# Kernel tuning notes

Measured on AMD Instinct MI355X. Metric: run time of the kernel, lower is better.

Reference implementation:

```python
import jax, jax.numpy as jnp
import numpy as np
import math

EPS = 1e-8
DIM, HEADS, K = 256, 8, 16
HD = DIM // HEADS
B, N, PDIM = 4, 4096, 3


def _layernorm(x, w, b, eps=1e-5):
    m = jnp.mean(x, axis=-1, keepdims=True)
    v = jnp.mean((x - m) ** 2, axis=-1, keepdims=True)
    return (x - m) * jax.lax.rsqrt(v + eps) * w + b


def setup_inputs() -> dict:
    key = jax.random.key(0)
    ks = jax.random.split(key, 16)
    s = 0.02
    d = {
        'x': jax.random.normal(ks[0], (B, N, DIM), jnp.float32),
        'positions': jax.random.uniform(ks[1], (B, N, PDIM), jnp.float32) * 0.5,  # inside unit ball
        'c': jnp.ones((1,), jnp.float32),
        'time_emb': jax.random.normal(ks[2], (B, DIM), jnp.float32),
        'Wq': jax.random.normal(ks[3], (DIM, DIM), jnp.float32) * s,
        'bq': jnp.zeros((DIM,), jnp.float32),
        'Wk': jax.random.normal(ks[4], (DIM, DIM), jnp.float32) * s,
        'bk': jnp.zeros((DIM,), jnp.float32),
        'Wv': jax.random.normal(ks[5], (DIM, DIM), jnp.float32) * s,
        'bv': jnp.zeros((DIM,), jnp.float32),
        'Wo': jax.random.normal(ks[6], (DIM, DIM), jnp.float32) * s,
        'bo': jnp.zeros((DIM,), jnp.float32),
        'W1': jax.random.normal(ks[7], (DIM, 4 * DIM), jnp.float32) * s,
        'b1': jnp.zeros((4 * DIM,), jnp.float32),
        'W2': jax.random.normal(ks[8], (4 * DIM, DIM), jnp.float32) * s,
        'b2': jnp.zeros((DIM,), jnp.float32),
        'ln1_w': jnp.ones((DIM,), jnp.float32),
        'ln1_b': jnp.zeros((DIM,), jnp.float32),
        'ln2_w': jnp.ones((DIM,), jnp.float32),
        'ln2_b': jnp.zeros((DIM,), jnp.float32),
        'log_tau': jnp.zeros((), jnp.float32),
    }
    return d


def _poincare_dist_matrix(pos, c):
    # pos: [B,N,P], c: scalar > 0. Returns [B,N,N] with d[b,i,j] = dist(pos[b,j], pos[b,i])
    sq = jnp.sum(pos ** 2, axis=-1)                      # [B,N]
    diff2 = (sq[:, :, None] + sq[:, None, :]
             - 2.0 * jnp.einsum('bip,bjp->bij', pos, pos))
    diff2 = jnp.maximum(diff2, 0.0)
    num = 2.0 * c * diff2
    den = (1.0 - c * sq[:, :, None]) * (1.0 - c * sq[:, None, :])
    arg = jnp.maximum(1.0 + num / (den + EPS), 1.0)
    return jnp.arccosh(arg) / jnp.sqrt(c)


def reference(x, positions, c, time_emb, Wq, bq, Wk, bk, Wv, bv, Wo, bo,
              W1, b1, W2, b2, ln1_w, ln1_b, ln2_w, ln2_b, log_tau):
    c_s = jnp.squeeze(c)
    x_res = x
    h = _layernorm(x, ln1_w, ln1_b) + time_emb[:, None, :]

    q = (h @ Wq + bq).reshape(B, N, HEADS, HD).transpose(0, 2, 1, 3)  # [B,H,N,hd]
    k = (h @ Wk + bk).reshape(B, N, HEADS, HD).transpose(0, 2, 1, 3)
    v = (h @ Wv + bv).reshape(B, N, HEADS, HD).transpose(0, 2, 1, 3)

    # pairwise hyperbolic distances + kNN (no_grad in original)
    dist = jax.lax.stop_gradient(_poincare_dist_matrix(positions, c_s))  # [B,N,N]
    neg_vals, idx = jax.lax.top_k(-dist, K)          # smallest-K distances
    attn_dists = -neg_vals                            # [B,N,K]

    # gather neighbor keys/values: out[b,h,n,j,d] = k[b,h,idx[b,n,j],d]
    idx_flat = idx.reshape(B, 1, N * K, 1)            # broadcast over heads, hd
    k_g = jnp.take_along_axis(k, idx_flat, axis=2).reshape(B, HEADS, N, K, HD)
    v_g = jnp.take_along_axis(v, idx_flat, axis=2).reshape(B, HEADS, N, K, HD)

    feat = jnp.einsum('bhnd,bhnkd->bhnk', q, k_g) / math.sqrt(HD)
    tau = jnp.exp(log_tau) + EPS
    scores = feat - attn_dists[:, None, :, :] / tau
    probs = jax.nn.softmax(scores, axis=-1)
    attn = jnp.einsum('bhnk,bhnkd->bhnd', probs, v_g)
    attn = attn.transpose(0, 2, 1, 3).reshape(B, N, DIM)

    x2 = x_res + attn @ Wo + bo
    ff = jax.nn.gelu(_layernorm(x2, ln2_w, ln2_b) @ W1 + b1, approximate=False) @ W2 + b2
    return x2 + ff
```

## Files before the change

kernel.cpp:

```cpp
#include <hip/hip_runtime.h>
#include <math.h>

namespace {

constexpr int kBatch = 4;
constexpr int kN = 4096;
constexpr int kDim = 256;
constexpr int kHeads = 8;
constexpr int kK = 16;
constexpr float kEps = 1e-8f;

using u16 = unsigned short;
typedef __attribute__((ext_vector_type(8))) short short8;
typedef __attribute__((ext_vector_type(8))) u16 u16x8;
typedef __attribute__((ext_vector_type(4))) float f32x4;

__device__ __forceinline__ float b2f(u16 u) {
  union { unsigned int i; float f; } x; x.i = ((unsigned int)u) << 16; return x.f;
}
__device__ __forceinline__ u16 f2b(float f) {
  union { float f; unsigned int i; } x; x.f = f;
  unsigned int r = x.i + 0x7fffu + ((x.i >> 16) & 1u);
  return (u16)(r >> 16);
}
__device__ __forceinline__ float gelu_exact(float x) {
  return 0.5f * x * (1.0f + erff(x * 0.70710678118654752f));
}
__device__ __forceinline__ void load_lds16(const u16* g, u16* l) {
  __builtin_amdgcn_global_load_lds(
      (const __attribute__((address_space(1))) unsigned int*)g,
      (__attribute__((address_space(3))) unsigned int*)l, 16, 0, 0);
}

template<bool ADD_TEMB>
__global__ __launch_bounds__(256) void ln_kernel(
    const float* __restrict__ x, const float* __restrict__ w,
    const float* __restrict__ bb, const float* __restrict__ temb,
    u16* __restrict__ out) {
  int gt = blockIdx.x * 256 + threadIdx.x;
  int row = gt >> 6;
  int lane = threadIdx.x & 63;
  const float4* xr = (const float4*)(x + (size_t)row * kDim);
  float4 v = xr[lane];
  float s = v.x + v.y + v.z + v.w;
  #pragma unroll
  for (int off = 32; off; off >>= 1) s += __shfl_xor(s, off);
  float mean = s * (1.0f / kDim);
  float dx = v.x - mean, dy = v.y - mean, dz = v.z - mean, dw = v.w - mean;
  float ss = dx * dx + dy * dy + dz * dz + dw * dw;
  #pragma unroll
  for (int off = 32; off; off >>= 1) ss += __shfl_xor(ss, off);
  float rstd = rsqrtf(ss * (1.0f / kDim) + 1e-5f);
  float4 wv = ((const float4*)w)[lane];
  float4 bv = ((const float4*)bb)[lane];
  float ox = dx * rstd * wv.x + bv.x;
  float oy = dy * rstd * wv.y + bv.y;
  float oz = dz * rstd * wv.z + bv.z;
  float ow = dw * rstd * wv.w + bv.w;
  if (ADD_TEMB) {
    int bi = row >> 12;
    float4 t = ((const float4*)(temb + (size_t)bi * kDim))[lane];
    ox += t.x; oy += t.y; oz += t.z; ow += t.w;
  }
  ushort4 ob;
  ob.x = f2b(ox); ob.y = f2b(oy); ob.z = f2b(oz); ob.w = f2b(ow);
  ((ushort4*)(out + (size_t)row * kDim))[lane] = ob;
}

__global__ __launch_bounds__(256) void wtrans_kernel(
    const float* __restrict__ Wq, const float* __restrict__ Wk,
    const float* __restrict__ Wv, const float* __restrict__ Wo,
    const float* __restrict__ W1, const float* __restrict__ W2,
    u16* __restrict__ Tq, u16* __restrict__ Tk,
    u16* __restrict__ Tv, u16* __restrict__ To,
    u16* __restrict__ T1, u16* __restrict__ T2) {
  __shared__ float t[32][33];
  int bx = blockIdx.x;
  int seg = bx >> 8, e = bx & 255;
  const float* W; u16* T; int Kin, Nin, kt, nt;
  if (seg == 0) {
    int which = e >> 6, tl = e & 63;
    W = which == 0 ? Wq : which == 1 ? Wk : which == 2 ? Wv : Wo;
    T = which == 0 ? Tq : which == 1 ? Tk : which == 2 ? Tv : To;
    Kin = 256; Nin = 256; kt = tl >> 3; nt = tl & 7;
  } else if (seg == 1) {
    W = W1; T = T1; Kin = 256; Nin = 1024; kt = e >> 5; nt = e & 31;
  } else {
    W = W2; T = T2; Kin = 1024; Nin = 256; kt = e >> 3; nt = e & 7;
  }
  int tx = threadIdx.x & 31, ty = threadIdx.x >> 5;
  #pragma unroll
  for (int rr = 0; rr < 4; ++rr) {
    int r = rr * 8 + ty;
    t[r][tx] = W[(size_t)(kt * 32 + r) * Nin + nt * 32 + tx];
  }
  __syncthreads();
  #pragma unroll
  for (int rr = 0; rr < 4; ++rr) {
    int r = rr * 8 + ty;
    T[(size_t)(nt * 32 + r) * Kin + kt * 32 + tx] = f2b(t[tx][r]);
  }
}

template<int EPI, int BN>
__device__ __forceinline__ void gemm_body(
    const u16* __restrict__ A, const u16* __restrict__ Bt,
    const float* __restrict__ bias, const float* __restrict__ R,
    float* __restrict__ Cf, u16* __restrict__ Cbf,
    int N, int K, int bx, int by) {
  constexpr int NI = BN / 32;
  constexpr int BK = 64;
  __shared__ u16 Al[128 * BK];
  __shared__ u16 Bl[BN * BK];
  int tid = threadIdx.x;
  int wv = tid >> 6, ln = tid & 63;
  int wr = wv >> 1, wc = wv & 1;
  int lhi = ln >> 4, llo = ln & 15;
  int bm = bx * 128, bn = by * BN;

  f32x4 zero = {0.f, 0.f, 0.f, 0.f};
  f32x4 acc[4][NI];
  #pragma unroll
  for (int mi = 0; mi < 4; ++mi)
    #pragma unroll
    for (int ni = 0; ni < NI; ++ni) acc[mi][ni] = zero;

  for (int k0 = 0; k0 < K; k0 += BK) {
    if (k0) __syncthreads();
    #pragma unroll
    for (int i = 0; i < 128 * BK / (8 * 256); ++i) {
      int f = i * 256 + tid;
      int r = f >> 3, o = f & 7;
      load_lds16(A + (size_t)(bm + r) * K + k0 + ((o ^ (r & 7)) << 3),
                 &Al[(i * 256 + wv * 64) * 8]);
    }
    #pragma unroll
    for (int i = 0; i < BN * BK / (8 * 256); ++i) {
      int f = i * 256 + tid;
      int r = f >> 3, o = f & 7;
      load_lds16(Bt + (size_t)(bn + r) * K + k0 + ((o ^ (r & 7)) << 3),
                 &Bl[(i * 256 + wv * 64) * 8]);
    }
    __syncthreads();
    #pragma unroll
    for (int ks = 0; ks < BK; ks += 32) {
      short8 af[4], bf[NI];
      #pragma unroll
      for (int mi = 0; mi < 4; ++mi) {
        int row = wr * 64 + mi * 16 + llo;
        int oct = ((ks >> 3) + lhi) ^ (llo & 7);
        af[mi] = *(const short8*)&Al[row * BK + oct * 8];
      }
      #pragma unroll
      for (int ni = 0; ni < NI; ++ni) {
        int row = wc * (BN / 2) + ni * 16 + llo;
        int oct = ((ks >> 3) + lhi) ^ (llo & 7);
        bf[ni] = *(const short8*)&Bl[row * BK + oct * 8];
      }
      #pragma unroll
      for (int mi = 0; mi < 4; ++mi)
        #pragma unroll
        for (int ni = 0; ni < NI; ++ni)
          acc[mi][ni] = __builtin_amdgcn_mfma_f32_16x16x32_bf16(
              af[mi], bf[ni], acc[mi][ni], 0, 0, 0);
    }
  }

  #pragma unroll
  for (int mi = 0; mi < 4; ++mi) {
    #pragma unroll
    for (int r = 0; r < 4; ++r) {
      int row = bm + wr * 64 + mi * 16 + lhi * 4 + r;
      #pragma unroll
      for (int ni = 0; ni < NI; ++ni) {
        int col = bn + wc * (BN / 2) + ni * 16 + llo;
        float val = acc[mi][ni][r] + bias[col];
        if (EPI == 1) {
          val += R[(size_t)row * N + col];
          Cf[(size_t)row * N + col] = val;
        } else {
          if (EPI == 2) val = gelu_exact(val);
          Cbf[(size_t)row * N + col] = f2b(val);
        }
      }
    }
  }
}

template<int EPI, int BN>
__global__ __launch_bounds__(256) void gemm_kernel(
    const u16* __restrict__ A, const u16* __restrict__ Bt,
    const float* __restrict__ bias, const float* __restrict__ R,
    float* __restrict__ Cf, u16* __restrict__ Cbf, int N, int K) {
  gemm_body<EPI, BN>(A, Bt, bias, R, Cf, Cbf, N, K, blockIdx.x, blockIdx.y);
}

__global__ __launch_bounds__(256) void qkv_kernel(
    const u16* __restrict__ A,
    const u16* __restrict__ Bq, const u16* __restrict__ Bk, const u16* __restrict__ Bv,
    const float* __restrict__ bq, const float* __restrict__ bk, const float* __restrict__ bv,
    u16* __restrict__ q, u16* __restrict__ k, u16* __restrict__ v) {
  int sel = blockIdx.y >> 1;
  const u16* Bt = sel == 0 ? Bq : sel == 1 ? Bk : Bv;
  const float* bias = sel == 0 ? bq : sel == 1 ? bk : bv;
  u16* C = sel == 0 ? q : sel == 1 ? k : v;
  gemm_body<0, 128>(A, Bt, bias, nullptr, nullptr, C, 256, 256,
                    blockIdx.x, blockIdx.y & 1);
}

__global__ __launch_bounds__(1024, 4) void topk_kernel(
    const float* __restrict__ pos, const float* __restrict__ cptr,
    int* __restrict__ idx_out, float* __restrict__ dist_out) {
  __shared__ float4 ps[kN];
  int tid = threadIdx.x;
  int wave = tid >> 6, ln = tid & 63;
  int row = blockIdx.x * 16 + wave;
  int b = row >> 12;
  float c = cptr[0];
  const float* pb = pos + (size_t)b * kN * 3;
  for (int j = tid; j < kN; j += 1024) {
    float x = pb[j * 3 + 0], y = pb[j * 3 + 1], z = pb[j * 3 + 2];
    ps[j] = make_float4(x, y, z, c * (x * x + y * y + z * z));
  }
  __syncthreads();

  int i = row & (kN - 1);
  float4 pi = ps[i];
  float wi = pi.w, oi = 1.0f - wi;
  float sx = 2.0f * c * pi.x, sy = 2.0f * c * pi.y, sz = 2.0f * c * pi.z;

  auto numden = [&](int j, float& num, float& den) {
    float4 pj = ps[j];
    float tt = wi + pj.w;
    tt = fmaf(-sx, pj.x, tt);
    tt = fmaf(-sy, pj.y, tt);
    tt = fmaf(-sz, pj.z, tt);
    num = fmaxf(tt, 0.0f);
    den = fmaf(-oi, pj.w, oi);
  };
  auto packkey = [&](float num, float den, int j) -> unsigned {
    float r = num * __builtin_amdgcn_rcpf(den);
    union { float f; unsigned u; } cv; cv.f = r;
    return (cv.u & 0xFFFFF000u) | (unsigned)j;
  };
  auto inflate = [&](unsigned T) -> float {
    union { unsigned u; float f; } tv; tv.u = T & 0xFFFFF000u;
    return fmaf(tv.f, 0.001f, tv.f);
  };

  float n0, d0;
  numden(ln, n0, d0);
  unsigned lpk = packkey(n0, d0, ln);
  #pragma unroll
  for (int kk = 2; kk <= 64; kk <<= 1) {
    #pragma unroll
    for (int jj = kk >> 1; jj >= 1; jj >>= 1) {
      unsigned ov = (unsigned)__shfl_xor((int)lpk, jj);
      bool keepMin = (((ln & kk) == 0) == ((ln & jj) == 0));
      bool less = ov < lpk;
      if (keepMin ? less : !less) lpk = ov;
    }
  }
  float Tf = inflate((unsigned)__builtin_amdgcn_readlane((int)lpk, 15));

  auto processGroup = [&](float num, float den, int base) {
    unsigned long long m = __ballot(num < Tf * den);
    if (m) {
      unsigned cpk = packkey(num, den, base + ln);
      do {
        int src = __ffsll(m) - 1;
        m &= m - 1;
        unsigned npk = (unsigned)__builtin_amdgcn_readlane((int)cpk, src);
        unsigned pv = (unsigned)__builtin_amdgcn_update_dpp(
            0, (int)lpk, 0x111 , 0xF, 0xF, false);
        bool gt = lpk > npk;
        bool take = gt && ((ln == 0) || (pv <= npk));
        lpk = take ? npk : (gt ? pv : lpk);
      } while (m);
      Tf = inflate((unsigned)__builtin_amdgcn_readlane((int)lpk, 15));
    }
  };

  int t = 1;
  for (; t + 3 < 64; t += 4) {
    float a0, b0, a1, b1, a2, b2, a3, b3;
    numden(ln + (t + 0) * 64, a0, b0);
    numden(ln + (t + 1) * 64, a1, b1);
    numden(ln + (t + 2) * 64, a2, b2);
    numden(ln + (t + 3) * 64, a3, b3);
    processGroup(a0, b0, (t + 0) * 64);
    processGroup(a1, b1, (t + 1) * 64);
    processGroup(a2, b2, (t + 2) * 64);
    processGroup(a3, b3, (t + 3) * 64);
  }
  for (; t < 64; ++t) {
    float a0, b0;
    numden(ln + t * 64, a0, b0);
    processGroup(a0, b0, t * 64);
  }

  if (ln < kK) {
    int j = (int)(lpk & 0xFFFu);
    float4 pj = ps[j];
    float tt = wi + pj.w;
    tt = fmaf(-sx, pj.x, tt);
    tt = fmaf(-sy, pj.y, tt);
    tt = fmaf(-sz, pj.z, tt);
    float num = 2.0f * fmaxf(tt, 0.0f);
    float den = fmaf(-oi, pj.w, oi) + kEps;
    float arg = fmaxf(1.0f + num / den, 1.0f);
    float rs = 1.0f / sqrtf(c);
    idx_out[(size_t)row * kK + ln] = j;
    dist_out[(size_t)row * kK + ln] = acoshf(arg) * rs;
  }
}

__global__ __launch_bounds__(256) void attn_kernel(
    const u16* __restrict__ q, const u16* __restrict__ k,
    const u16* __restrict__ v, const int* __restrict__ nidx,
    const float* __restrict__ ndist, const float* __restrict__ log_tau,
    u16* __restrict__ out) {
  int t = blockIdx.x * 256 + threadIdx.x;
  int h = t & (kHeads - 1);
  int row = t >> 3;
  int b = row >> 12;
  float rtau = 1.0f / (expf(log_tau[0]) + kEps);
  const u16x8* qr = (const u16x8*)(q + (size_t)row * kDim + h * 32);
  float qf[32];
  #pragma unroll
  for (int cch = 0; cch < 4; ++cch) {
    u16x8 u = qr[cch];
    #pragma unroll
    for (int e = 0; e < 8; ++e) qf[cch * 8 + e] = b2f(u[e]);
  }

  int njs[kK];
  float sc[kK];
  const int* ir = nidx + (size_t)row * kK;
  const float* dr = ndist + (size_t)row * kK;
  float smax = -1e30f;
  #pragma unroll
  for (int j = 0; j < kK; ++j) {
    int nj = ir[j];
    njs[j] = nj;
    const u16x8* kr = (const u16x8*)(k + ((size_t)b * kN + nj) * kDim + h * 32);
    float dot = 0.0f;
    #pragma unroll
    for (int cch = 0; cch < 4; ++cch) {
      u16x8 u = kr[cch];
      #pragma unroll
      for (int e = 0; e < 8; ++e) dot = fmaf(qf[cch * 8 + e], b2f(u[e]), dot);
    }
    float s = dot * 0.17677669529663687f - dr[j] * rtau;
    sc[j] = s;
    smax = fmaxf(smax, s);
  }
  float sum = 0.0f;
  #pragma unroll
  for (int j = 0; j < kK; ++j) { sc[j] = expf(sc[j] - smax); sum += sc[j]; }
  float rsum = 1.0f / sum;
  float o[32];
  #pragma unroll
  for (int d = 0; d < 32; ++d) o[d] = 0.0f;
  #pragma unroll
  for (int j = 0; j < kK; ++j) {
    float p = sc[j] * rsum;
    const u16x8* vr = (const u16x8*)(v + ((size_t)b * kN + njs[j]) * kDim + h * 32);
    #pragma unroll
    for (int cch = 0; cch < 4; ++cch) {
      u16x8 u = vr[cch];
      #pragma unroll
      for (int e = 0; e < 8; ++e) o[cch * 8 + e] = fmaf(p, b2f(u[e]), o[cch * 8 + e]);
    }
  }
  u16x8* orow = (u16x8*)(out + (size_t)row * kDim + h * 32);
  #pragma unroll
  for (int cch = 0; cch < 4; ++cch) {
    u16x8 po;
    #pragma unroll
    for (int e = 0; e < 8; ++e) po[e] = f2b(o[cch * 8 + e]);
    orow[cch] = po;
  }
}

}

extern "C" void kernel_launch(void* const* d_in, const int* in_sizes, int n_in,
                              void* d_out, int out_size, void* d_ws, size_t ws_size,
                              hipStream_t stream) {
  const float* x    = (const float*)d_in[0];
  const float* pos  = (const float*)d_in[1];
  const float* c    = (const float*)d_in[2];
  const float* temb = (const float*)d_in[3];
  const float* Wq   = (const float*)d_in[4];
  const float* bq   = (const float*)d_in[5];
  const float* Wk   = (const float*)d_in[6];
  const float* bk   = (const float*)d_in[7];
  const float* Wv   = (const float*)d_in[8];
  const float* bv   = (const float*)d_in[9];
  const float* Wo   = (const float*)d_in[10];
  const float* bo   = (const float*)d_in[11];
  const float* W1   = (const float*)d_in[12];
  const float* b1   = (const float*)d_in[13];
  const float* W2   = (const float*)d_in[14];
  const float* b2   = (const float*)d_in[15];
  const float* ln1w = (const float*)d_in[16];
  const float* ln1b = (const float*)d_in[17];
  const float* ln2w = (const float*)d_in[18];
  const float* ln2b = (const float*)d_in[19];
  const float* ltau = (const float*)d_in[20];

  const size_t MB = 1ull << 20;
  char* w = (char*)d_ws;
  u16*   h_bf  = (u16*)(w + 0 * MB);
  u16*   qb    = (u16*)(w + 8 * MB);
  u16*   kb    = (u16*)(w + 16 * MB);
  u16*   vb    = (u16*)(w + 24 * MB);
  u16*   attnb = (u16*)(w + 32 * MB);
  float* x2    = (float*)(w + 40 * MB);
  u16*   g_bf  = (u16*)(w + 56 * MB);
  u16*   wq_t  = (u16*)(w + 88 * MB);
  u16*   wk_t  = wq_t + 65536;
  u16*   wv_t  = wq_t + 2 * 65536;
  u16*   wo_t  = wq_t + 3 * 65536;
  u16*   w1_t  = (u16*)(w + 89 * MB);
  u16*   w2_t  = (u16*)(w + 89 * MB + 512 * 1024);
  int*   kidx  = (int*)(w + 90 * MB);
  float* kdst  = (float*)(w + 91 * MB);
  u16*   tln   = h_bf;

  hipLaunchKernelGGL(wtrans_kernel, dim3(768), dim3(256), 0, stream,
                     Wq, Wk, Wv, Wo, W1, W2, wq_t, wk_t, wv_t, wo_t, w1_t, w2_t);
  hipLaunchKernelGGL((ln_kernel<true>), dim3(4096), dim3(256), 0, stream,
                     x, ln1w, ln1b, temb, h_bf);
  hipLaunchKernelGGL(topk_kernel, dim3(1024), dim3(1024), 0, stream,
                     pos, c, kidx, kdst);
  hipLaunchKernelGGL(qkv_kernel, dim3(128, 6), dim3(256), 0, stream,
                     h_bf, wq_t, wk_t, wv_t, bq, bk, bv, qb, kb, vb);
  hipLaunchKernelGGL(attn_kernel, dim3(512), dim3(256), 0, stream,
                     qb, kb, vb, kidx, kdst, ltau, attnb);
  hipLaunchKernelGGL((gemm_kernel<1, 64>), dim3(128, 4), dim3(256), 0, stream,
                     attnb, wo_t, bo, x, x2, (u16*)nullptr, 256, 256);
  hipLaunchKernelGGL((ln_kernel<false>), dim3(4096), dim3(256), 0, stream,
                     x2, ln2w, ln2b, nullptr, tln);
  hipLaunchKernelGGL((gemm_kernel<2, 128>), dim3(128, 8), dim3(256), 0, stream,
                     tln, w1_t, b1, nullptr, (float*)nullptr, g_bf, 1024, 256);
  hipLaunchKernelGGL((gemm_kernel<1, 64>), dim3(128, 4), dim3(256), 0, stream,
                     g_bf, w2_t, b2, x2, (float*)d_out, (u16*)nullptr, 256, 1024);
}
```

Measured before the change: 179.9 us.

## Merge LN1 into weight-prep kernel and streamline top-k threshold test

Folds the first layernorm into the weight-transpose launch, using extra blocks to save one kernel launch. In top-k, the candidate test num < T*den is rewritten algebraically as one FMA chain against a precomputed right-hand side. Four ballots are batched so the threshold is refreshed only once per group of four. The sorted-insert step is simplified to a min/max select. The later threshold refresh may let slightly more candidates through, but the insertion stays exact.

```diff
diff --git a/kernel.cpp b/kernel.cpp
--- a/kernel.cpp
+++ b/kernel.cpp
@@ -33,13 +33,12 @@
 }
 
 template<bool ADD_TEMB>
-__global__ __launch_bounds__(256) void ln_kernel(
+__device__ __forceinline__ void ln_body(
     const float* __restrict__ x, const float* __restrict__ w,
     const float* __restrict__ bb, const float* __restrict__ temb,
-    u16* __restrict__ out) {
-  int gt = blockIdx.x * 256 + threadIdx.x;
+    u16* __restrict__ out, int gt) {
   int row = gt >> 6;
-  int lane = threadIdx.x & 63;
+  int lane = gt & 63;
   const float4* xr = (const float4*)(x + (size_t)row * kDim);
   float4 v = xr[lane];
   float s = v.x + v.y + v.z + v.w;
@@ -67,7 +66,18 @@
   ((ushort4*)(out + (size_t)row * kDim))[lane] = ob;
 }
 
-__global__ __launch_bounds__(256) void wtrans_kernel(
+template<bool ADD_TEMB>
+__global__ __launch_bounds__(256) void ln_kernel(
+    const float* __restrict__ x, const float* __restrict__ w,
+    const float* __restrict__ bb, const float* __restrict__ temb,
+    u16* __restrict__ out) {
+  ln_body<ADD_TEMB>(x, w, bb, temb, out, blockIdx.x * 256 + threadIdx.x);
+}
+
+__global__ __launch_bounds__(256) void prep_kernel(
+    const float* __restrict__ x, const float* __restrict__ ln1w,
+    const float* __restrict__ ln1b, const float* __restrict__ temb,
+    u16* __restrict__ h_out,
     const float* __restrict__ Wq, const float* __restrict__ Wk,
     const float* __restrict__ Wv, const float* __restrict__ Wo,
     const float* __restrict__ W1, const float* __restrict__ W2,
@@ -76,6 +86,10 @@
     u16* __restrict__ T1, u16* __restrict__ T2) {
   __shared__ float t[32][33];
   int bx = blockIdx.x;
+  if (bx >= 768) {
+    ln_body<true>(x, ln1w, ln1b, temb, h_out, (bx - 768) * 256 + threadIdx.x);
+    return;
+  }
   int seg = bx >> 8, e = bx & 255;
   const float* W; u16* T; int Kin, Nin, kt, nt;
   if (seg == 0) {
@@ -229,15 +243,6 @@
   float wi = pi.w, oi = 1.0f - wi;
   float sx = 2.0f * c * pi.x, sy = 2.0f * c * pi.y, sz = 2.0f * c * pi.z;
 
-  auto numden = [&](int j, float& num, float& den) {
-    float4 pj = ps[j];
-    float tt = wi + pj.w;
-    tt = fmaf(-sx, pj.x, tt);
-    tt = fmaf(-sy, pj.y, tt);
-    tt = fmaf(-sz, pj.z, tt);
-    num = fmaxf(tt, 0.0f);
-    den = fmaf(-oi, pj.w, oi);
-  };
   auto packkey = [&](float num, float den, int j) -> unsigned {
     float r = num * __builtin_amdgcn_rcpf(den);
     union { float f; unsigned u; } cv; cv.f = r;
@@ -248,9 +253,17 @@
     return fmaf(tv.f, 0.001f, tv.f);
   };
 
-  float n0, d0;
-  numden(ln, n0, d0);
-  unsigned lpk = packkey(n0, d0, ln);
+  unsigned lpk;
+  {
+    float4 pj = ps[ln];
+    float tt = wi + pj.w;
+    tt = fmaf(-sx, pj.x, tt);
+    tt = fmaf(-sy, pj.y, tt);
+    tt = fmaf(-sz, pj.z, tt);
+    float num = fmaxf(tt, 0.0f);
+    float den = fmaf(-oi, pj.w, oi);
+    lpk = packkey(num, den, ln);
+  }
   #pragma unroll
   for (int kk = 2; kk <= 64; kk <<= 1) {
     #pragma unroll
@@ -262,41 +275,60 @@
     }
   }
   float Tf = inflate((unsigned)__builtin_amdgcn_readlane((int)lpk, 15));
-
-  auto processGroup = [&](float num, float den, int base) {
-    unsigned long long m = __ballot(num < Tf * den);
-    if (m) {
-      unsigned cpk = packkey(num, den, base + ln);
-      do {
-        int src = __ffsll(m) - 1;
-        m &= m - 1;
-        unsigned npk = (unsigned)__builtin_amdgcn_readlane((int)cpk, src);
-        unsigned pv = (unsigned)__builtin_amdgcn_update_dpp(
-            0, (int)lpk, 0x111 , 0xF, 0xF, false);
-        bool gt = lpk > npk;
-        bool take = gt && ((ln == 0) || (pv <= npk));
-        lpk = take ? npk : (gt ? pv : lpk);
-      } while (m);
-      Tf = inflate((unsigned)__builtin_amdgcn_readlane((int)lpk, 15));
-    }
+  float qq = fmaf(Tf, oi, 1.0f);
+  float rhs = fmaf(-Tf, oi, wi);
+
+  auto score = [&](const float4& pj) {
+    return fmaf(pj.x, sx, fmaf(pj.y, sy, fmaf(pj.z, sz, pj.w * (-qq))));
+  };
+  auto insertMask = [&](unsigned long long m, const float4& pj, int base) {
+    float tt = wi + pj.w;
+    tt = fmaf(-sx, pj.x, tt);
+    tt = fmaf(-sy, pj.y, tt);
+    tt = fmaf(-sz, pj.z, tt);
+    float num = fmaxf(tt, 0.0f);
+    float den = fmaf(-oi, pj.w, oi);
+    unsigned cpk = packkey(num, den, base + ln);
+    do {
+      int src = __ffsll(m) - 1;
+      m &= m - 1;
+      unsigned npk = (unsigned)__builtin_amdgcn_readlane((int)cpk, src);
+      unsigned pv = (unsigned)__builtin_amdgcn_update_dpp(
+          0, (int)lpk, 0x111 , 0xF, 0xF, false);
+      unsigned mx = pv > npk ? pv : npk;
+      lpk = mx < lpk ? mx : lpk;
+    } while (m);
+  };
+  auto refresh = [&]() {
+    Tf = inflate((unsigned)__builtin_amdgcn_readlane((int)lpk, 15));
+    qq = fmaf(Tf, oi, 1.0f);
+    rhs = fmaf(-Tf, oi, wi);
   };
 
   int t = 1;
   for (; t + 3 < 64; t += 4) {
-    float a0, b0, a1, b1, a2, b2, a3, b3;
-    numden(ln + (t + 0) * 64, a0, b0);
-    numden(ln + (t + 1) * 64, a1, b1);
-    numden(ln + (t + 2) * 64, a2, b2);
-    numden(ln + (t + 3) * 64, a3, b3);
-    processGroup(a0, b0, (t + 0) * 64);
-    processGroup(a1, b1, (t + 1) * 64);
-    processGroup(a2, b2, (t + 2) * 64);
-    processGroup(a3, b3, (t + 3) * 64);
+    float4 p0 = ps[ln + (t + 0) * 64];
+    float4 p1 = ps[ln + (t + 1) * 64];
+    float4 p2 = ps[ln + (t + 2) * 64];
+    float4 p3 = ps[ln + (t + 3) * 64];
+    float a0 = score(p0), a1 = score(p1), a2 = score(p2), a3 = score(p3);
+    unsigned long long m0 = __ballot(a0 > rhs);
+    unsigned long long m1 = __ballot(a1 > rhs);
+    unsigned long long m2 = __ballot(a2 > rhs);
+    unsigned long long m3 = __ballot(a3 > rhs);
+    if (m0 | m1 | m2 | m3) {
+      if (m0) insertMask(m0, p0, (t + 0) * 64);
+      if (m1) insertMask(m1, p1, (t + 1) * 64);
+      if (m2) insertMask(m2, p2, (t + 2) * 64);
+      if (m3) insertMask(m3, p3, (t + 3) * 64);
+      refresh();
+    }
   }
   for (; t < 64; ++t) {
-    float a0, b0;
-    numden(ln + t * 64, a0, b0);
-    processGroup(a0, b0, t * 64);
+    float4 p0 = ps[ln + t * 64];
+    float a0 = score(p0);
+    unsigned long long m0 = __ballot(a0 > rhs);
+    if (m0) { insertMask(m0, p0, t * 64); refresh(); }
   }
 
   if (ln < kK) {
@@ -429,10 +461,9 @@
   float* kdst  = (float*)(w + 91 * MB);
   u16*   tln   = h_bf;
 
-  hipLaunchKernelGGL(wtrans_kernel, dim3(768), dim3(256), 0, stream,
+  hipLaunchKernelGGL(prep_kernel, dim3(4864), dim3(256), 0, stream,
+                     x, ln1w, ln1b, temb, h_bf,
                      Wq, Wk, Wv, Wo, W1, W2, wq_t, wk_t, wv_t, wo_t, w1_t, w2_t);
-  hipLaunchKernelGGL((ln_kernel<true>), dim3(4096), dim3(256), 0, stream,
-                     x, ln1w, ln1b, temb, h_bf);
   hipLaunchKernelGGL(topk_kernel, dim3(1024), dim3(1024), 0, stream,
                      pos, c, kidx, kdst);
   hipLaunchKernelGGL(qkv_kernel, dim3(128, 6), dim3(256), 0, stream,
```

After: 180.5 us. Within noise of the previous version (+0.3%).

## Merge weight transpose, LN1 and top-k into one launch; fuse Wo GEMM with LN2

Applied to the files above, without the earlier changes.

Weight transpose, the first layernorm and the kNN top-k now run as one heterogeneous grid, with block ranges dispatched to each task. The Wo projection GEMM is fused with the residual add and the second layernorm. A 64-row by 256-column tile gives each block full rows, so row statistics are reduced through LDS. This removes three launches and the x2 write-then-reread between the Wo GEMM and LN2. In exchange, the front kernel's launch bound drops from 4 to 2 blocks per SM, which may lower top-k occupancy. The fused LN2 also uses the E[x^2]-mean^2 variance formula and a grid of only 256 blocks.

```diff
diff --git a/kernel.cpp b/kernel.cpp
--- a/kernel.cpp
+++ b/kernel.cpp
@@ -33,13 +33,12 @@
 }
 
 template<bool ADD_TEMB>
-__global__ __launch_bounds__(256) void ln_kernel(
+__device__ __forceinline__ void ln_body(
     const float* __restrict__ x, const float* __restrict__ w,
     const float* __restrict__ bb, const float* __restrict__ temb,
-    u16* __restrict__ out) {
-  int gt = blockIdx.x * 256 + threadIdx.x;
+    u16* __restrict__ out, int gt) {
   int row = gt >> 6;
-  int lane = threadIdx.x & 63;
+  int lane = gt & 63;
   const float4* xr = (const float4*)(x + (size_t)row * kDim);
   float4 v = xr[lane];
   float s = v.x + v.y + v.z + v.w;
@@ -67,160 +66,65 @@
   ((ushort4*)(out + (size_t)row * kDim))[lane] = ob;
 }
 
-__global__ __launch_bounds__(256) void wtrans_kernel(
+__global__ __launch_bounds__(1024, 2) void front_kernel(
+    const float* __restrict__ pos, const float* __restrict__ cptr,
+    int* __restrict__ idx_out, float* __restrict__ dist_out,
+    const float* __restrict__ x, const float* __restrict__ ln1w,
+    const float* __restrict__ ln1b, const float* __restrict__ temb,
+    u16* __restrict__ h_out,
     const float* __restrict__ Wq, const float* __restrict__ Wk,
     const float* __restrict__ Wv, const float* __restrict__ Wo,
     const float* __restrict__ W1, const float* __restrict__ W2,
     u16* __restrict__ Tq, u16* __restrict__ Tk,
     u16* __restrict__ Tv, u16* __restrict__ To,
     u16* __restrict__ T1, u16* __restrict__ T2) {
-  __shared__ float t[32][33];
-  int bx = blockIdx.x;
-  int seg = bx >> 8, e = bx & 255;
-  const float* W; u16* T; int Kin, Nin, kt, nt;
-  if (seg == 0) {
-    int which = e >> 6, tl = e & 63;
-    W = which == 0 ? Wq : which == 1 ? Wk : which == 2 ? Wv : Wo;
-    T = which == 0 ? Tq : which == 1 ? Tk : which == 2 ? Tv : To;
-    Kin = 256; Nin = 256; kt = tl >> 3; nt = tl & 7;
-  } else if (seg == 1) {
-    W = W1; T = T1; Kin = 256; Nin = 1024; kt = e >> 5; nt = e & 31;
-  } else {
-    W = W2; T = T2; Kin = 1024; Nin = 256; kt = e >> 3; nt = e & 7;
-  }
-  int tx = threadIdx.x & 31, ty = threadIdx.x >> 5;
-  #pragma unroll
-  for (int rr = 0; rr < 4; ++rr) {
-    int r = rr * 8 + ty;
-    t[r][tx] = W[(size_t)(kt * 32 + r) * Nin + nt * 32 + tx];
-  }
-  __syncthreads();
-  #pragma unroll
-  for (int rr = 0; rr < 4; ++rr) {
-    int r = rr * 8 + ty;
-    T[(size_t)(nt * 32 + r) * Kin + kt * 32 + tx] = f2b(t[tx][r]);
-  }
-}
-
-template<int EPI, int BN>
-__device__ __forceinline__ void gemm_body(
-    const u16* __restrict__ A, const u16* __restrict__ Bt,
-    const float* __restrict__ bias, const float* __restrict__ R,
-    float* __restrict__ Cf, u16* __restrict__ Cbf,
-    int N, int K, int bx, int by) {
-  constexpr int NI = BN / 32;
-  constexpr int BK = 64;
-  __shared__ u16 Al[128 * BK];
-  __shared__ u16 Bl[BN * BK];
-  int tid = threadIdx.x;
-  int wv = tid >> 6, ln = tid & 63;
-  int wr = wv >> 1, wc = wv & 1;
-  int lhi = ln >> 4, llo = ln & 15;
-  int bm = bx * 128, bn = by * BN;
-
-  f32x4 zero = {0.f, 0.f, 0.f, 0.f};
-  f32x4 acc[4][NI];
-  #pragma unroll
-  for (int mi = 0; mi < 4; ++mi)
-    #pragma unroll
-    for (int ni = 0; ni < NI; ++ni) acc[mi][ni] = zero;
-
-  for (int k0 = 0; k0 < K; k0 += BK) {
-    if (k0) __syncthreads();
-    #pragma unroll
-    for (int i = 0; i < 128 * BK / (8 * 256); ++i) {
-      int f = i * 256 + tid;
-      int r = f >> 3, o = f & 7;
-      load_lds16(A + (size_t)(bm + r) * K + k0 + ((o ^ (r & 7)) << 3),
-                 &Al[(i * 256 + wv * 64) * 8]);
-    }
-    #pragma unroll
-    for (int i = 0; i < BN * BK / (8 * 256); ++i) {
-      int f = i * 256 + tid;
-      int r = f >> 3, o = f & 7;
-      load_lds16(Bt + (size_t)(bn + r) * K + k0 + ((o ^ (r & 7)) << 3),
-                 &Bl[(i * 256 + wv * 64) * 8]);
-    }
-    __syncthreads();
-    #pragma unroll
-    for (int ks = 0; ks < BK; ks += 32) {
-      short8 af[4], bf[NI];
-      #pragma unroll
-      for (int mi = 0; mi < 4; ++mi) {
-        int row = wr * 64 + mi * 16 + llo;
-        int oct = ((ks >> 3) + lhi) ^ (llo & 7);
-        af[mi] = *(const short8*)&Al[row * BK + oct * 8];
-      }
-      #pragma unroll
-      for (int ni = 0; ni < NI; ++ni) {
-        int row = wc * (BN / 2) + ni * 16 + llo;
-        int oct = ((ks >> 3) + lhi) ^ (llo & 7);
-        bf[ni] = *(const short8*)&Bl[row * BK + oct * 8];
-      }
-      #pragma unroll
-      for (int mi = 0; mi < 4; ++mi)
-        #pragma unroll
-        for (int ni = 0; ni < NI; ++ni)
-          acc[mi][ni] = __builtin_amdgcn_mfma_f32_16x16x32_bf16(
-              af[mi], bf[ni], acc[mi][ni], 0, 0, 0);
-    }
-  }
-
-  #pragma unroll
-  for (int mi = 0; mi < 4; ++mi) {
-    #pragma unroll
-    for (int r = 0; r < 4; ++r) {
-      int row = bm + wr * 64 + mi * 16 + lhi * 4 + r;
-      #pragma unroll
-      for (int ni = 0; ni < NI; ++ni) {
-        int col = bn + wc * (BN / 2) + ni * 16 + llo;
-        float val = acc[mi][ni][r] + bias[col];
-        if (EPI == 1) {
-          val += R[(size_t)row * N + col];
-          Cf[(size_t)row * N + col] = val;
-        } else {
-          if (EPI == 2) val = gelu_exact(val);
-          Cbf[(size_t)row * N + col] = f2b(val);
-        }
-      }
-    }
-  }
-}
-
-template<int EPI, int BN>
-__global__ __launch_bounds__(256) void gemm_kernel(
-    const u16* __restrict__ A, const u16* __restrict__ Bt,
-    const float* __restrict__ bias, const float* __restrict__ R,
-    float* __restrict__ Cf, u16* __restrict__ Cbf, int N, int K) {
-  gemm_body<EPI, BN>(A, Bt, bias, R, Cf, Cbf, N, K, blockIdx.x, blockIdx.y);
-}
-
-__global__ __launch_bounds__(256) void qkv_kernel(
-    const u16* __restrict__ A,
-    const u16* __restrict__ Bq, const u16* __restrict__ Bk, const u16* __restrict__ Bv,
-    const float* __restrict__ bq, const float* __restrict__ bk, const float* __restrict__ bv,
-    u16* __restrict__ q, u16* __restrict__ k, u16* __restrict__ v) {
-  int sel = blockIdx.y >> 1;
-  const u16* Bt = sel == 0 ? Bq : sel == 1 ? Bk : Bv;
-  const float* bias = sel == 0 ? bq : sel == 1 ? bk : bv;
-  u16* C = sel == 0 ? q : sel == 1 ? k : v;
-  gemm_body<0, 128>(A, Bt, bias, nullptr, nullptr, C, 256, 256,
-                    blockIdx.x, blockIdx.y & 1);
-}
-
-__global__ __launch_bounds__(1024, 4) void topk_kernel(
-    const float* __restrict__ pos, const float* __restrict__ cptr,
-    int* __restrict__ idx_out, float* __restrict__ dist_out) {
   __shared__ float4 ps[kN];
   int tid = threadIdx.x;
+  int bx = blockIdx.x;
+
+  if (bx >= 1024) {
+    if (bx < 1216) {
+      int sub = tid >> 8, stid = tid & 255;
+      int task = (bx - 1024) * 4 + sub;
+      float* tt = (float*)ps + sub * 1056;
+      int seg = task >> 8, e = task & 255;
+      const float* W; u16* T; int Kin, Nin, kt, nt;
+      if (seg == 0) {
+        int which = e >> 6, tl = e & 63;
+        W = which == 0 ? Wq : which == 1 ? Wk : which == 2 ? Wv : Wo;
+        T = which == 0 ? Tq : which == 1 ? Tk : which == 2 ? Tv : To;
+        Kin = 256; Nin = 256; kt = tl >> 3; nt = tl & 7;
+      } else if (seg == 1) {
+        W = W1; T = T1; Kin = 256; Nin = 1024; kt = e >> 5; nt = e & 31;
+      } else {
+        W = W2; T = T2; Kin = 1024; Nin = 256; kt = e >> 3; nt = e & 7;
+      }
+      int tx = stid & 31, ty = stid >> 5;
+      #pragma unroll
+      for (int rr = 0; rr < 4; ++rr) {
+        int r = rr * 8 + ty;
+        tt[r * 33 + tx] = W[(size_t)(kt * 32 + r) * Nin + nt * 32 + tx];
+      }
+      __syncthreads();
+      #pragma unroll
+      for (int rr = 0; rr < 4; ++rr) {
+        int r = rr * 8 + ty;
+        T[(size_t)(nt * 32 + r) * Kin + kt * 32 + tx] = f2b(tt[tx * 33 + r]);
+      }
+    } else {
+      ln_body<true>(x, ln1w, ln1b, temb, h_out, (bx - 1216) * 1024 + tid);
+    }
+    return;
+  }
+
   int wave = tid >> 6, ln = tid & 63;
-  int row = blockIdx.x * 16 + wave;
+  int row = bx * 16 + wave;
   int b = row >> 12;
   float c = cptr[0];
   const float* pb = pos + (size_t)b * kN * 3;
   for (int j = tid; j < kN; j += 1024) {
-    float x = pb[j * 3 + 0], y = pb[j * 3 + 1], z = pb[j * 3 + 2];
-    ps[j] = make_float4(x, y, z, c * (x * x + y * y + z * z));
+    float px = pb[j * 3 + 0], py = pb[j * 3 + 1], pz = pb[j * 3 + 2];
+    ps[j] = make_float4(px, py, pz, c * (px * px + py * py + pz * pz));
   }
   __syncthreads();
 
@@ -312,6 +216,229 @@
     float rs = 1.0f / sqrtf(c);
     idx_out[(size_t)row * kK + ln] = j;
     dist_out[(size_t)row * kK + ln] = acoshf(arg) * rs;
+  }
+}
+
+template<int EPI, int BN>
+__device__ __forceinline__ void gemm_body(
+    const u16* __restrict__ A, const u16* __restrict__ Bt,
+    const float* __restrict__ bias, const float* __restrict__ R,
+    float* __restrict__ Cf, u16* __restrict__ Cbf,
+    int N, int K, int bx, int by) {
+  constexpr int NI = BN / 32;
+  constexpr int BK = 64;
+  __shared__ u16 Al[128 * BK];
+  __shared__ u16 Bl[BN * BK];
+  int tid = threadIdx.x;
+  int wv = tid >> 6, ln = tid & 63;
+  int wr = wv >> 1, wc = wv & 1;
+  int lhi = ln >> 4, llo = ln & 15;
+  int bm = bx * 128, bn = by * BN;
+
+  f32x4 zero = {0.f, 0.f, 0.f, 0.f};
+  f32x4 acc[4][NI];
+  #pragma unroll
+  for (int mi = 0; mi < 4; ++mi)
+    #pragma unroll
+    for (int ni = 0; ni < NI; ++ni) acc[mi][ni] = zero;
+
+  for (int k0 = 0; k0 < K; k0 += BK) {
+    if (k0) __syncthreads();
+    #pragma unroll
+    for (int i = 0; i < 128 * BK / (8 * 256); ++i) {
+      int f = i * 256 + tid;
+      int r = f >> 3, o = f & 7;
+      load_lds16(A + (size_t)(bm + r) * K + k0 + ((o ^ (r & 7)) << 3),
+                 &Al[(i * 256 + wv * 64) * 8]);
+    }
+    #pragma unroll
+    for (int i = 0; i < BN * BK / (8 * 256); ++i) {
+      int f = i * 256 + tid;
+      int r = f >> 3, o = f & 7;
+      load_lds16(Bt + (size_t)(bn + r) * K + k0 + ((o ^ (r & 7)) << 3),
+                 &Bl[(i * 256 + wv * 64) * 8]);
+    }
+    __syncthreads();
+    #pragma unroll
+    for (int ks = 0; ks < BK; ks += 32) {
+      short8 af[4], bf[NI];
+      #pragma unroll
+      for (int mi = 0; mi < 4; ++mi) {
+        int row = wr * 64 + mi * 16 + llo;
+        int oct = ((ks >> 3) + lhi) ^ (llo & 7);
+        af[mi] = *(const short8*)&Al[row * BK + oct * 8];
+      }
+      #pragma unroll
+      for (int ni = 0; ni < NI; ++ni) {
+        int row = wc * (BN / 2) + ni * 16 + llo;
+        int oct = ((ks >> 3) + lhi) ^ (llo & 7);
+        bf[ni] = *(const short8*)&Bl[row * BK + oct * 8];
+      }
+      #pragma unroll
+      for (int mi = 0; mi < 4; ++mi)
+        #pragma unroll
+        for (int ni = 0; ni < NI; ++ni)
+          acc[mi][ni] = __builtin_amdgcn_mfma_f32_16x16x32_bf16(
+              af[mi], bf[ni], acc[mi][ni], 0, 0, 0);
+    }
+  }
+
+  #pragma unroll
+  for (int mi = 0; mi < 4; ++mi) {
+    #pragma unroll
+    for (int r = 0; r < 4; ++r) {
+      int row = bm + wr * 64 + mi * 16 + lhi * 4 + r;
+      #pragma unroll
+      for (int ni = 0; ni < NI; ++ni) {
+        int col = bn + wc * (BN / 2) + ni * 16 + llo;
+        float val = acc[mi][ni][r] + bias[col];
+        if (EPI == 1) {
+          val += R[(size_t)row * N + col];
+          Cf[(size_t)row * N + col] = val;
+        } else {
+          if (EPI == 2) val = gelu_exact(val);
+          Cbf[(size_t)row * N + col] = f2b(val);
+        }
+      }
+    }
+  }
+}
+
+template<int EPI, int BN>
+__global__ __launch_bounds__(256) void gemm_kernel(
+    const u16* __restrict__ A, const u16* __restrict__ Bt,
+    const float* __restrict__ bias, const float* __restrict__ R,
+    float* __restrict__ Cf, u16* __restrict__ Cbf, int N, int K) {
+  gemm_body<EPI, BN>(A, Bt, bias, R, Cf, Cbf, N, K, blockIdx.x, blockIdx.y);
+}
+
+__global__ __launch_bounds__(256) void qkv_kernel(
+    const u16* __restrict__ A,
+    const u16* __restrict__ Bq, const u16* __restrict__ Bk, const u16* __restrict__ Bv,
+    const float* __restrict__ bq, const float* __restrict__ bk, const float* __restrict__ bv,
+    u16* __restrict__ q, u16* __restrict__ k, u16* __restrict__ v) {
+  int sel = blockIdx.y >> 1;
+  const u16* Bt = sel == 0 ? Bq : sel == 1 ? Bk : Bv;
+  const float* bias = sel == 0 ? bq : sel == 1 ? bk : bv;
+  u16* C = sel == 0 ? q : sel == 1 ? k : v;
+  gemm_body<0, 128>(A, Bt, bias, nullptr, nullptr, C, 256, 256,
+                    blockIdx.x, blockIdx.y & 1);
+}
+
+__global__ __launch_bounds__(512) void wo_ln_kernel(
+    const u16* __restrict__ A, const u16* __restrict__ Bt,
+    const float* __restrict__ bo, const float* __restrict__ xres,
+    const float* __restrict__ ln2w, const float* __restrict__ ln2b,
+    float* __restrict__ x2, u16* __restrict__ tln) {
+  __shared__ u16 Al[64 * 64];
+  __shared__ u16 Bl[256 * 64];
+  __shared__ float red[4][64][2];
+  int tid = threadIdx.x;
+  int wv = tid >> 6, ln = tid & 63;
+  int wr = wv >> 2, wc = wv & 3;
+  int lhi = ln >> 4, llo = ln & 15;
+  int bm = blockIdx.x * 64;
+
+  f32x4 zero = {0.f, 0.f, 0.f, 0.f};
+  f32x4 acc[2][4];
+  #pragma unroll
+  for (int mi = 0; mi < 2; ++mi)
+    #pragma unroll
+    for (int ni = 0; ni < 4; ++ni) acc[mi][ni] = zero;
+
+  for (int k0 = 0; k0 < 256; k0 += 64) {
+    if (k0) __syncthreads();
+    {
+      int f = tid, r = f >> 3, o = f & 7;
+      load_lds16(A + (size_t)(bm + r) * 256 + k0 + ((o ^ (r & 7)) << 3),
+                 &Al[(wv * 64) * 8]);
+    }
+    #pragma unroll
+    for (int i = 0; i < 4; ++i) {
+      int f = i * 512 + tid, r = f >> 3, o = f & 7;
+      load_lds16(Bt + (size_t)r * 256 + k0 + ((o ^ (r & 7)) << 3),
+                 &Bl[((i * 8 + wv) * 64) * 8]);
+    }
+    __syncthreads();
+    #pragma unroll
+    for (int ks = 0; ks < 64; ks += 32) {
+      short8 af[2], bf[4];
+      #pragma unroll
+      for (int mi = 0; mi < 2; ++mi) {
+        int row = wr * 32 + mi * 16 + llo;
+        int oct = ((ks >> 3) + lhi) ^ (llo & 7);
+        af[mi] = *(const short8*)&Al[row * 64 + oct * 8];
+      }
+      #pragma unroll
+      for (int ni = 0; ni < 4; ++ni) {
+        int brow = wc * 64 + ni * 16 + llo;
+        int oct = ((ks >> 3) + lhi) ^ (llo & 7);
+        bf[ni] = *(const short8*)&Bl[brow * 64 + oct * 8];
+      }
+      #pragma unroll
+      for (int mi = 0; mi < 2; ++mi)
+        #pragma unroll
+        for (int ni = 0; ni < 4; ++ni)
+          acc[mi][ni] = __builtin_amdgcn_mfma_f32_16x16x32_bf16(
+              af[mi], bf[ni], acc[mi][ni], 0, 0, 0);
+    }
+  }
+
+  float psum[2][4], psq[2][4];
+  #pragma unroll
+  for (int mi = 0; mi < 2; ++mi) {
+    #pragma unroll
+    for (int r = 0; r < 4; ++r) {
+      int row = bm + wr * 32 + mi * 16 + lhi * 4 + r;
+      float s = 0.0f, q = 0.0f;
+      #pragma unroll
+      for (int ni = 0; ni < 4; ++ni) {
+        int col = wc * 64 + ni * 16 + llo;
+        float v = acc[mi][ni][r] + bo[col] + xres[(size_t)row * 256 + col];
+        acc[mi][ni][r] = v;
+        s += v;
+        q = fmaf(v, v, q);
+      }
+      #pragma unroll
+      for (int off = 1; off < 16; off <<= 1) {
+        s += __shfl_xor(s, off);
+        q += __shfl_xor(q, off);
+      }
+      psum[mi][r] = s; psq[mi][r] = q;
+    }
+  }
+  if (llo == 0) {
+    #pragma unroll
+    for (int mi = 0; mi < 2; ++mi)
+      #pragma unroll
+      for (int r = 0; r < 4; ++r) {
+        int rl = wr * 32 + mi * 16 + lhi * 4 + r;
+        red[wc][rl][0] = psum[mi][r];
+        red[wc][rl][1] = psq[mi][r];
+      }
+  }
+  __syncthreads();
+  constexpr float rn = 1.0f / 256.0f;
+  #pragma unroll
+  for (int mi = 0; mi < 2; ++mi) {
+    #pragma unroll
+    for (int r = 0; r < 4; ++r) {
+      int rl = wr * 32 + mi * 16 + lhi * 4 + r;
+      int row = bm + rl;
+      float S = red[0][rl][0] + red[1][rl][0] + red[2][rl][0] + red[3][rl][0];
+      float Q = red[0][rl][1] + red[1][rl][1] + red[2][rl][1] + red[3][rl][1];
+      float mean = S * rn;
+      float var = Q * rn - mean * mean;
+      float rstd = rsqrtf(var + 1e-5f);
+      #pragma unroll
+      for (int ni = 0; ni < 4; ++ni) {
+        int col = wc * 64 + ni * 16 + llo;
+        float v = acc[mi][ni][r];
+        x2[(size_t)row * 256 + col] = v;
+        tln[(size_t)row * 256 + col] =
+            f2b((v - mean) * rstd * ln2w[col] + ln2b[col]);
+      }
+    }
   }
 }
 
@@ -429,20 +556,16 @@
   float* kdst  = (float*)(w + 91 * MB);
   u16*   tln   = h_bf;
 
-  hipLaunchKernelGGL(wtrans_kernel, dim3(768), dim3(256), 0, stream,
+  hipLaunchKernelGGL(front_kernel, dim3(2240), dim3(1024), 0, stream,
+                     pos, c, kidx, kdst,
+                     x, ln1w, ln1b, temb, h_bf,
                      Wq, Wk, Wv, Wo, W1, W2, wq_t, wk_t, wv_t, wo_t, w1_t, w2_t);
-  hipLaunchKernelGGL((ln_kernel<true>), dim3(4096), dim3(256), 0, stream,
-                     x, ln1w, ln1b, temb, h_bf);
-  hipLaunchKernelGGL(topk_kernel, dim3(1024), dim3(1024), 0, stream,
-                     pos, c, kidx, kdst);
   hipLaunchKernelGGL(qkv_kernel, dim3(128, 6), dim3(256), 0, stream,
                      h_bf, wq_t, wk_t, wv_t, bq, bk, bv, qb, kb, vb);
   hipLaunchKernelGGL(attn_kernel, dim3(512), dim3(256), 0, stream,
                      qb, kb, vb, kidx, kdst, ltau, attnb);
-  hipLaunchKernelGGL((gemm_kernel<1, 64>), dim3(128, 4), dim3(256), 0, stream,
-                     attnb, wo_t, bo, x, x2, (u16*)nullptr, 256, 256);
-  hipLaunchKernelGGL((ln_kernel<false>), dim3(4096), dim3(256), 0, stream,
-                     x2, ln2w, ln2b, nullptr, tln);
+  hipLaunchKernelGGL(wo_ln_kernel, dim3(256), dim3(512), 0, stream,
+                     attnb, wo_t, bo, x, ln2w, ln2b, x2, tln);
   hipLaunchKernelGGL((gemm_kernel<2, 128>), dim3(128, 8), dim3(256), 0, stream,
                      tln, w1_t, b1, nullptr, (float*)nullptr, g_bf, 1024, 256);
   hipLaunchKernelGGL((gemm_kernel<1, 64>), dim3(128, 4), dim3(256), 0, stream,
```

Result: faster. 165.1 us (-8.2%).
